# Performance work log

Hardware: AMD Instinct MI355X
Metric: run time of the kernel (lower is better)

## Reference

```python
import jax, jax.numpy as jnp
import numpy as np


def _pairwise_mse_gram(x):
    """G[i, j] = mean_d (x[i, d] - x[j, d])**2, computed in closed form.

    Replaces the original O(N^2) Python double loop over F.mse_loss with a
    single GEMM: |x_i|^2 + |x_j|^2 - 2 x_i . x_j, divided by D.
    """
    x = x.reshape(x.shape[0], -1)            # [N, D]
    D = x.shape[1]
    sq = jnp.sum(x * x, axis=1)              # [N]
    gram = x @ x.T                           # [N, N] GEMM
    return (sq[:, None] + sq[None, :] - 2.0 * gram) / D


def setup_inputs() -> dict:
    key = jax.random.key(0)
    k1, k2 = jax.random.split(key)
    fm_s = jax.random.normal(k1, (1024, 64, 16, 16), dtype=jnp.float32)
    fm_t = jax.random.normal(k2, (1024, 64, 16, 16), dtype=jnp.float32)
    return {"fm_s": fm_s, "fm_t": fm_t}


def reference(fm_s, fm_t):
    # Faithful to the original source, including its bug: the second double
    # loop writes the teacher pairwise-MSE matrix into G_s (overwriting the
    # student one entirely), while G_t stays all-zeros. Hence the final loss
    # is mse(pairwise_mse_gram(fm_t), 0) and fm_s does not affect the output.
    G_s = _pairwise_mse_gram(fm_t)           # [N, N]
    G_t = jnp.zeros_like(G_s)
    return jnp.mean((G_s - G_t) ** 2)
```

## Files before the change

kernel.cpp:

```cpp
#include <hip/hip_runtime.h>
#include <hip/hip_bf16.h>
#include <stdint.h>

#define N_ROWS 1024
#define KDIM   16384
#define BK     32
#define KCHUNKS (KDIM / BK)
#define SPLITS  25

#define XB_BYTES  ((size_t)N_ROWS * KDIM * 2)
#define SQ_BYTES  ((size_t)4096)
#define P_BYTES   ((size_t)10 * SPLITS * 65536 * 2)
#define WS_NEEDED (XB_BYTES + SQ_BYTES + P_BYTES)

typedef __attribute__((ext_vector_type(8))) __bf16 bf16x8;
typedef __attribute__((ext_vector_type(8))) unsigned short ushort8;
typedef __attribute__((ext_vector_type(4))) float  f32x4;

#define GLOBAL_AS __attribute__((address_space(1)))
#define LDS_AS    __attribute__((address_space(3)))

#define WAITCNT_VM(N) __builtin_amdgcn_s_waitcnt(0x0F70 | (N))

__device__ __forceinline__ void block_barrier() {
    asm volatile("" ::: "memory");
    __builtin_amdgcn_s_barrier();
    asm volatile("" ::: "memory");
}

__device__ __constant__ unsigned char T_I[10] = {0,0,0,0, 1,1,1, 2,2, 3};
__device__ __constant__ unsigned char T_J[10] = {0,1,2,3, 1,2,3, 2,3, 3};

__device__ __forceinline__ unsigned short f32_to_bf16_rne(float f) {
    unsigned int u = __float_as_uint(f);
    unsigned int lsb = (u >> 16) & 1u;
    u += 0x7fffu + lsb;
    return (unsigned short)(u >> 16);
}

__global__ __launch_bounds__(256) void cast_sq_kernel(
        const float* __restrict__ X, unsigned short* __restrict__ Xb,
        float* __restrict__ sq) {
    const int row = blockIdx.x >> 1;
    const int seg = blockIdx.x & 1;
    const float4* src = (const float4*)(X + (size_t)row * KDIM) + seg * 2048;
    uint2* dst = (uint2*)(Xb + (size_t)row * KDIM) + seg * 2048;
    float ss = 0.f;
#pragma unroll
    for (int c = 0; c < 8; ++c) {
        int idx = c * 256 + threadIdx.x;
        float4 v = src[idx];
        ss += v.x * v.x + v.y * v.y + v.z * v.z + v.w * v.w;
        uint2 p;
        p.x = (unsigned int)f32_to_bf16_rne(v.x) | ((unsigned int)f32_to_bf16_rne(v.y) << 16);
        p.y = (unsigned int)f32_to_bf16_rne(v.z) | ((unsigned int)f32_to_bf16_rne(v.w) << 16);
        dst[idx] = p;
    }
#pragma unroll
    for (int o = 32; o; o >>= 1) ss += __shfl_down(ss, o, 64);
    __shared__ float red[4];
    int lane = threadIdx.x & 63, wv = threadIdx.x >> 6;
    if (lane == 0) red[wv] = ss;
    __syncthreads();
    if (threadIdx.x == 0) atomicAdd(&sq[row], red[0] + red[1] + red[2] + red[3]);
}

__global__ __launch_bounds__(256, 1) void gram_gemm_kernel(
        const unsigned short* __restrict__ Xb, unsigned short* __restrict__ P) {
    __shared__ unsigned short SH[3 * 16384];

    const int row0 = T_I[blockIdx.x] * 256;
    const int col0 = T_J[blockIdx.x] * 256;
    const int cs = (blockIdx.y * KCHUNKS) / SPLITS;
    const int ce = ((blockIdx.y + 1) * KCHUNKS) / SPLITS;
    const int niter = ce - cs;

    const int tid  = threadIdx.x;
    const int lane = tid & 63;
    const int wv   = tid >> 6;
    const int wm   = (wv >> 1) * 128;
    const int wn   = (wv & 1) * 128;
    const int lr   = lane & 15;
    const int lq   = lane >> 4;
    const int soff = (lq ^ ((lr >> 1) & 3)) * 8;

    const unsigned short* gA[4];
    const unsigned short* gB[4];
#pragma unroll
    for (int it = 0; it < 4; ++it) {
        int c = it * 256 + tid;
        int r = c >> 2;
        int js = (c & 3) ^ ((r >> 1) & 3);
        gA[it] = Xb + (size_t)(row0 + r) * KDIM + cs * BK + js * 8;
        gB[it] = Xb + (size_t)(col0 + r) * KDIM + cs * BK + js * 8;
    }

    f32x4 acc[8][8] = {};

#define STAGE(ph, kk)                                                          \
    do {                                                                       \
        unsigned short* b = &SH[(ph) * 16384];                                 \
        _Pragma("unroll")                                                      \
        for (int it = 0; it < 4; ++it) {                                       \
            int c = it * 256 + tid;                                            \
            __builtin_amdgcn_global_load_lds((GLOBAL_AS void*)(void*)(gA[it] + (kk)), \
                                             (LDS_AS void*)&b[c * 8], 16, 0, 0);      \
            __builtin_amdgcn_global_load_lds((GLOBAL_AS void*)(void*)(gB[it] + (kk)), \
                                             (LDS_AS void*)&b[8192 + c * 8], 16, 0, 0); \
        }                                                                      \
    } while (0)

#define COMPUTE(ph)                                                            \
    do {                                                                       \
        const unsigned short* b = &SH[(ph) * 16384];                           \
        bf16x8 af[8], bq[8];                                                   \
        _Pragma("unroll")                                                      \
        for (int i = 0; i < 8; ++i)                                            \
            af[i] = *(const bf16x8*)&b[(wm + i * 16 + lr) * 32 + soff];        \
        _Pragma("unroll")                                                      \
        for (int j = 0; j < 8; ++j)                                            \
            bq[j] = *(const bf16x8*)&b[8192 + (wn + j * 16 + lr) * 32 + soff]; \
        _Pragma("unroll")                                                      \
        for (int i = 0; i < 8; ++i)                                            \
            _Pragma("unroll")                                                  \
            for (int j = 0; j < 8; ++j)                                        \
                acc[i][j] = __builtin_amdgcn_mfma_f32_16x16x32_bf16(           \
                    af[i], bq[j], acc[i][j], 0, 0, 0);                         \
    } while (0)

    STAGE(0, 0);
    STAGE(1, BK);

    int cph = 0, wph = 2;
    for (int k = 0; k < niter; ++k) {
        if (k < niter - 1) WAITCNT_VM(8);
        else               WAITCNT_VM(0);
        block_barrier();
        if (k + 2 < niter) STAGE(wph, (k + 2) * BK);
        COMPUTE(cph);
        cph = (cph == 2) ? 0 : cph + 1;
        wph = (wph == 2) ? 0 : wph + 1;
    }
#undef STAGE
#undef COMPUTE

    unsigned short* dst = P + ((size_t)blockIdx.x * SPLITS + blockIdx.y) * 65536;
    const int rbase = wm + lq * 4;
    const int cbase = wn + lr;
#pragma unroll
    for (int i = 0; i < 8; ++i)
#pragma unroll
        for (int j = 0; j < 8; ++j)
#pragma unroll
            for (int r = 0; r < 4; ++r) {
                int e = (rbase + i * 16 + r) * 256 + (cbase + j * 16);
                dst[e] = f32_to_bf16_rne(acc[i][j][r]);
            }
}

__global__ __launch_bounds__(256) void loss_kernel(
        const unsigned short* __restrict__ P, const float* __restrict__ sq,
        float* __restrict__ out) {
    const float invD = 1.0f / (float)KDIM;
    const int u  = blockIdx.x * 256 + threadIdx.x;
    const int t  = u >> 13;
    const int e0 = (u & 8191) * 8;

    const unsigned short* pb = P + (size_t)t * SPLITS * 65536 + e0;
    float g[8] = {};
#pragma unroll
    for (int s = 0; s < SPLITS; ++s) {
        ushort8 v = *(const ushort8*)(pb + (size_t)s * 65536);
#pragma unroll
        for (int x = 0; x < 8; ++x)
            g[x] += __uint_as_float(((unsigned int)v[x]) << 16);
    }
    const int i  = T_I[t] * 256 + (e0 >> 8);
    const int jb = T_J[t] * 256 + (e0 & 255);
    const float w = (T_I[t] == T_J[t]) ? 1.0f : 2.0f;
    const float sqi = sq[i];
    float acc = 0.f;
#pragma unroll
    for (int x = 0; x < 8; ++x) {
        float v = (sqi + sq[jb + x] - 2.0f * g[x]) * invD;
        acc += w * v * v;
    }
#pragma unroll
    for (int o = 32; o; o >>= 1) acc += __shfl_down(acc, o, 64);
    __shared__ float red[4];
    int lane = threadIdx.x & 63, wv = threadIdx.x >> 6;
    if (lane == 0) red[wv] = acc;
    __syncthreads();
    if (threadIdx.x == 0) {
        float total = red[0] + red[1] + red[2] + red[3];
        atomicAdd(out, total * (1.0f / ((float)N_ROWS * (float)N_ROWS)));
    }
}

extern "C" void kernel_launch(void* const* d_in, const int* in_sizes, int n_in,
                              void* d_out, int out_size, void* d_ws, size_t ws_size,
                              hipStream_t stream) {
    const float* fm_t = (const float*)d_in[1];
    float* out = (float*)d_out;

    char* ws = (char*)d_ws;
    unsigned short* Xb = (unsigned short*)ws;
    float* sq = (float*)(ws + XB_BYTES);

    unsigned short* P = (ws_size >= WS_NEEDED)
        ? (unsigned short*)(ws + XB_BYTES + SQ_BYTES)
        : (unsigned short*)d_in[0];

    hipMemsetAsync(out, 0, sizeof(float), stream);
    hipMemsetAsync(sq, 0, N_ROWS * sizeof(float), stream);

    cast_sq_kernel<<<dim3(2 * N_ROWS), 256, 0, stream>>>(fm_t, Xb, sq);
    gram_gemm_kernel<<<dim3(10, SPLITS), 256, 0, stream>>>(Xb, P);
    loss_kernel<<<dim3(320), 256, 0, stream>>>(P, sq, out);
}
```

Measured before the change: 173.0 us.

## Switch Gram GEMM to 32x32x16 MFMA and drop memsets via per-segment norms

The GEMM inner loop now uses 32x32x16 bf16 MFMA tiles (a 4x4 grid of 16-wide accumulators per wave) in place of 16x16x32 tiles. This cuts the number of MFMA issues and LDS fragment loads per k-step, and the LDS read addresses and the epilogue row mapping are adjusted to match. Separately, the two hipMemsetAsync calls are removed: the cast kernel zeroes the output itself and writes one partial squared norm per half-row instead of using atomics, and the loss kernel adds the two halves together. This trims launch overhead, but the zeroing of out now depends on the cast kernel running before the loss kernel.

```diff
diff --git a/kernel.cpp b/kernel.cpp
--- a/kernel.cpp
+++ b/kernel.cpp
@@ -9,13 +9,13 @@
 #define SPLITS  25
 
 #define XB_BYTES  ((size_t)N_ROWS * KDIM * 2)
-#define SQ_BYTES  ((size_t)4096)
+#define SQ_BYTES  ((size_t)8192)
 #define P_BYTES   ((size_t)10 * SPLITS * 65536 * 2)
 #define WS_NEEDED (XB_BYTES + SQ_BYTES + P_BYTES)
 
-typedef __attribute__((ext_vector_type(8))) __bf16 bf16x8;
-typedef __attribute__((ext_vector_type(8))) unsigned short ushort8;
-typedef __attribute__((ext_vector_type(4))) float  f32x4;
+typedef __attribute__((ext_vector_type(8)))  __bf16 bf16x8;
+typedef __attribute__((ext_vector_type(8)))  unsigned short ushort8;
+typedef __attribute__((ext_vector_type(16))) float  f32x16;
 
 #define GLOBAL_AS __attribute__((address_space(1)))
 #define LDS_AS    __attribute__((address_space(3)))
@@ -40,7 +40,8 @@
 
 __global__ __launch_bounds__(256) void cast_sq_kernel(
         const float* __restrict__ X, unsigned short* __restrict__ Xb,
-        float* __restrict__ sq) {
+        float* __restrict__ sq2, float* __restrict__ out) {
+    if (blockIdx.x == 0 && threadIdx.x == 0) out[0] = 0.f;
     const int row = blockIdx.x >> 1;
     const int seg = blockIdx.x & 1;
     const float4* src = (const float4*)(X + (size_t)row * KDIM) + seg * 2048;
@@ -62,7 +63,7 @@
     int lane = threadIdx.x & 63, wv = threadIdx.x >> 6;
     if (lane == 0) red[wv] = ss;
     __syncthreads();
-    if (threadIdx.x == 0) atomicAdd(&sq[row], red[0] + red[1] + red[2] + red[3]);
+    if (threadIdx.x == 0) sq2[blockIdx.x] = red[0] + red[1] + red[2] + red[3];
 }
 
 __global__ __launch_bounds__(256, 1) void gram_gemm_kernel(
@@ -80,9 +81,8 @@
     const int wv   = tid >> 6;
     const int wm   = (wv >> 1) * 128;
     const int wn   = (wv & 1) * 128;
-    const int lr   = lane & 15;
-    const int lq   = lane >> 4;
-    const int soff = (lq ^ ((lr >> 1) & 3)) * 8;
+    const int lr   = lane & 31;
+    const int lq   = lane >> 5;
 
     const unsigned short* gA[4];
     const unsigned short* gB[4];
@@ -95,7 +95,7 @@
         gB[it] = Xb + (size_t)(col0 + r) * KDIM + cs * BK + js * 8;
     }
 
-    f32x4 acc[8][8] = {};
+    f32x16 acc[4][4] = {};
 
 #define STAGE(ph, kk)                                                          \
     do {                                                                       \
@@ -113,19 +113,32 @@
 #define COMPUTE(ph)                                                            \
     do {                                                                       \
         const unsigned short* b = &SH[(ph) * 16384];                           \
-        bf16x8 af[8], bq[8];                                                   \
-        _Pragma("unroll")                                                      \
-        for (int i = 0; i < 8; ++i)                                            \
-            af[i] = *(const bf16x8*)&b[(wm + i * 16 + lr) * 32 + soff];        \
-        _Pragma("unroll")                                                      \
-        for (int j = 0; j < 8; ++j)                                            \
-            bq[j] = *(const bf16x8*)&b[8192 + (wn + j * 16 + lr) * 32 + soff]; \
-        _Pragma("unroll")                                                      \
-        for (int i = 0; i < 8; ++i)                                            \
+        bf16x8 af[4][2], bq[4][2];                                             \
+        _Pragma("unroll")                                                      \
+        for (int i = 0; i < 4; ++i)                                            \
             _Pragma("unroll")                                                  \
-            for (int j = 0; j < 8; ++j)                                        \
-                acc[i][j] = __builtin_amdgcn_mfma_f32_16x16x32_bf16(           \
-                    af[i], bq[j], acc[i][j], 0, 0, 0);                         \
+            for (int s = 0; s < 2; ++s) {                                      \
+                int ra = wm + i * 32 + lr;                                     \
+                af[i][s] = *(const bf16x8*)&b[ra * 32 +                        \
+                    ((s * 2 + lq) ^ ((ra >> 1) & 3)) * 8];                     \
+            }                                                                  \
+        _Pragma("unroll")                                                      \
+        for (int j = 0; j < 4; ++j)                                            \
+            _Pragma("unroll")                                                  \
+            for (int s = 0; s < 2; ++s) {                                      \
+                int rb = wn + j * 32 + lr;                                     \
+                bq[j][s] = *(const bf16x8*)&b[8192 + rb * 32 +                 \
+                    ((s * 2 + lq) ^ ((rb >> 1) & 3)) * 8];                     \
+            }                                                                  \
+        _Pragma("unroll")                                                      \
+        for (int i = 0; i < 4; ++i)                                            \
+            _Pragma("unroll")                                                  \
+            for (int j = 0; j < 4; ++j) {                                      \
+                acc[i][j] = __builtin_amdgcn_mfma_f32_32x32x16_bf16(           \
+                    af[i][0], bq[j][0], acc[i][j], 0, 0, 0);                   \
+                acc[i][j] = __builtin_amdgcn_mfma_f32_32x32x16_bf16(           \
+                    af[i][1], bq[j][1], acc[i][j], 0, 0, 0);                   \
+            }                                                                  \
     } while (0)
 
     STAGE(0, 0);
@@ -145,21 +158,22 @@
 #undef COMPUTE
 
     unsigned short* dst = P + ((size_t)blockIdx.x * SPLITS + blockIdx.y) * 65536;
-    const int rbase = wm + lq * 4;
+    const int rq = 4 * lq;
     const int cbase = wn + lr;
 #pragma unroll
-    for (int i = 0; i < 8; ++i)
-#pragma unroll
-        for (int j = 0; j < 8; ++j)
-#pragma unroll
-            for (int r = 0; r < 4; ++r) {
-                int e = (rbase + i * 16 + r) * 256 + (cbase + j * 16);
-                dst[e] = f32_to_bf16_rne(acc[i][j][r]);
+    for (int i = 0; i < 4; ++i)
+#pragma unroll
+        for (int j = 0; j < 4; ++j)
+#pragma unroll
+            for (int t = 0; t < 16; ++t) {
+                int row = wm + i * 32 + (t & 3) + 8 * (t >> 2) + rq;
+                int e = row * 256 + (cbase + j * 32);
+                dst[e] = f32_to_bf16_rne(acc[i][j][t]);
             }
 }
 
 __global__ __launch_bounds__(256) void loss_kernel(
-        const unsigned short* __restrict__ P, const float* __restrict__ sq,
+        const unsigned short* __restrict__ P, const float* __restrict__ sq2,
         float* __restrict__ out) {
     const float invD = 1.0f / (float)KDIM;
     const int u  = blockIdx.x * 256 + threadIdx.x;
@@ -175,14 +189,17 @@
         for (int x = 0; x < 8; ++x)
             g[x] += __uint_as_float(((unsigned int)v[x]) << 16);
     }
+    const float2* sqp = (const float2*)sq2;
     const int i  = T_I[t] * 256 + (e0 >> 8);
     const int jb = T_J[t] * 256 + (e0 & 255);
     const float w = (T_I[t] == T_J[t]) ? 1.0f : 2.0f;
-    const float sqi = sq[i];
+    const float2 si = sqp[i];
+    const float sqi = si.x + si.y;
     float acc = 0.f;
 #pragma unroll
     for (int x = 0; x < 8; ++x) {
-        float v = (sqi + sq[jb + x] - 2.0f * g[x]) * invD;
+        float2 sj = sqp[jb + x];
+        float v = (sqi + (sj.x + sj.y) - 2.0f * g[x]) * invD;
         acc += w * v * v;
     }
 #pragma unroll
@@ -205,16 +222,13 @@
 
     char* ws = (char*)d_ws;
     unsigned short* Xb = (unsigned short*)ws;
-    float* sq = (float*)(ws + XB_BYTES);
+    float* sq2 = (float*)(ws + XB_BYTES);
 
     unsigned short* P = (ws_size >= WS_NEEDED)
         ? (unsigned short*)(ws + XB_BYTES + SQ_BYTES)
         : (unsigned short*)d_in[0];
 
-    hipMemsetAsync(out, 0, sizeof(float), stream);
-    hipMemsetAsync(sq, 0, N_ROWS * sizeof(float), stream);
-
-    cast_sq_kernel<<<dim3(2 * N_ROWS), 256, 0, stream>>>(fm_t, Xb, sq);
+    cast_sq_kernel<<<dim3(2 * N_ROWS), 256, 0, stream>>>(fm_t, Xb, sq2, out);
     gram_gemm_kernel<<<dim3(10, SPLITS), 256, 0, stream>>>(Xb, P);
-    loss_kernel<<<dim3(320), 256, 0, stream>>>(P, sq, out);
-}
+    loss_kernel<<<dim3(320), 256, 0, stream>>>(P, sq2, out);
+}
```

Measured after the change: 168.4 us. -2.6%, faster.
